# Performance work log

Hardware: AMD Instinct MI355X
Metric: run time of the kernel (lower is better)

The kernel has to match this reference:

```python
import jax, jax.numpy as jnp
import numpy as np

MAX_MARKER = 16


def setup_inputs() -> dict:
    key = jax.random.key(0)
    ks = jax.random.split(key, 7)
    B, W, H = 65536, 512, 8
    s1 = 1.0 / np.sqrt(W)
    s2 = 1.0 / np.sqrt(H)
    return {
        "x": jax.random.normal(ks[0], (B, W), dtype=jnp.float32),
        "W1": jax.random.uniform(ks[1], (H, W), jnp.float32, -s1, s1),
        "b1": jax.random.uniform(ks[2], (H,), jnp.float32, -s1, s1),
        "W2": jax.random.uniform(ks[3], (H, H), jnp.float32, -s2, s2),
        "b2": jax.random.uniform(ks[4], (H,), jnp.float32, -s2, s2),
        "W3": jax.random.uniform(ks[5], (W, H), jnp.float32, -s2, s2),
        "b3": jax.random.uniform(ks[6], (W,), jnp.float32, -s2, s2),
    }


def reference(x, W1, b1, W2, b2, W3, b3):
    # tiny MLP: window -> 8 -> 8 -> window
    h = jax.nn.relu(x @ W1.T + b1)
    h = jax.nn.relu(h @ W2.T + b2)
    y = h @ W3.T + b3
    p = jax.nn.softmax(y, axis=1)
    # force endpoints on (x.data[:,0]=1; x.data[:,-1]=1)
    p = p.at[:, 0].set(1.0).at[:, -1].set(1.0)
    # top-k along dim 1; threshold = min of the top-k values per row
    top_vals, _ = jax.lax.top_k(p, MAX_MARKER)
    thr = top_vals[:, -1:]  # sorted desc -> last is min, shape [B,1]
    # binary mask writes: >= thr -> 1, else 0
    return jnp.where(p >= thr, 1.0, 0.0).astype(p.dtype)
```

## Files before the change

kernel.cpp:

```cpp
#include <hip/hip_runtime.h>
#include <math.h>

#define B_ROWS 65536
#define WDIM 512
#define HDIM 8
#define THREADS 512

typedef float native_float4 __attribute__((ext_vector_type(4)));

template<int CTRL, int ROWM>
__device__ __forceinline__ float dpp_mov(float oldv, float x) {
    return __int_as_float(__builtin_amdgcn_update_dpp(
        __float_as_int(oldv), __float_as_int(x), CTRL, ROWM, 0xF, false));
}

__device__ __forceinline__ float wave_sum(float x) {
    x += dpp_mov<0x121, 0xF>(0.f, x);
    x += dpp_mov<0x122, 0xF>(0.f, x);
    x += dpp_mov<0x124, 0xF>(0.f, x);
    x += dpp_mov<0x128, 0xF>(0.f, x);
    x += dpp_mov<0x142, 0xA>(0.f, x);
    x += dpp_mov<0x143, 0xC>(0.f, x);
    return __int_as_float(__builtin_amdgcn_readlane(__float_as_int(x), 63));
}

__device__ __forceinline__ float wave_max(float x) {
    x = fmaxf(x, dpp_mov<0x121, 0xF>(-INFINITY, x));
    x = fmaxf(x, dpp_mov<0x122, 0xF>(-INFINITY, x));
    x = fmaxf(x, dpp_mov<0x124, 0xF>(-INFINITY, x));
    x = fmaxf(x, dpp_mov<0x128, 0xF>(-INFINITY, x));
    x = fmaxf(x, dpp_mov<0x142, 0xA>(-INFINITY, x));
    x = fmaxf(x, dpp_mov<0x143, 0xC>(-INFINITY, x));
    return __int_as_float(__builtin_amdgcn_readlane(__float_as_int(x), 63));
}

__device__ __forceinline__ float dot8(native_float4 a0, native_float4 a1,
                                      native_float4 b0, native_float4 b1) {
    float s = a0.x * b0.x;
    s = fmaf(a0.y, b0.y, s); s = fmaf(a0.z, b0.z, s); s = fmaf(a0.w, b0.w, s);
    s = fmaf(a1.x, b1.x, s); s = fmaf(a1.y, b1.y, s);
    s = fmaf(a1.z, b1.z, s); s = fmaf(a1.w, b1.w, s);
    return s;
}

__global__ __launch_bounds__(THREADS, 2)
void fused_mlp_topk(const float* __restrict__ x,
                    const float* __restrict__ W1,
                    const float* __restrict__ b1,
                    const float* __restrict__ W2,
                    const float* __restrict__ b2,
                    const float* __restrict__ W3,
                    const float* __restrict__ b3,
                    float* __restrict__ out)
{
    __shared__ __align__(16) float sW1[HDIM * WDIM];
    __shared__ __align__(16) float sW3t[HDIM * WDIM];
    __shared__ __align__(16) float sb3[WDIM];

    const int tid = threadIdx.x;
    for (int i = tid; i < HDIM * WDIM; i += THREADS) sW1[i] = W1[i];
    for (int i = tid; i < HDIM * WDIM; i += THREADS) {
        int r = i >> 3, k = i & 7;
        sW3t[k * WDIM + r] = W3[i];
    }
    for (int i = tid; i < WDIM; i += THREADS) sb3[i] = b3[i];
    __syncthreads();

    const int lane = tid & 63;
    const int wave_id = blockIdx.x * (THREADS / 64) + (tid >> 6);

    const native_float4* sW1v = reinterpret_cast<const native_float4*>(sW1);
    const native_float4* sW3v = reinterpret_cast<const native_float4*>(sW3t);
    const native_float4* sb3v = reinterpret_cast<const native_float4*>(sb3);

    int ra = wave_id * 2;
    const native_float4* xpa = reinterpret_cast<const native_float4*>(x + (size_t)ra * WDIM);
    const native_float4* xpb = xpa + (WDIM / 4);
    native_float4 xa0 = __builtin_nontemporal_load(xpa + lane);
    native_float4 xa1 = __builtin_nontemporal_load(xpa + lane + 64);
    native_float4 xb0 = __builtin_nontemporal_load(xpb + lane);
    native_float4 xb1 = __builtin_nontemporal_load(xpb + lane + 64);

    #pragma unroll 1
    for (int it = 0; it < 4; ++it) {
        float pa[HDIM], pb[HDIM];
        #pragma unroll
        for (int j = 0; j < HDIM; ++j) {
            native_float4 w0 = sW1v[j * 128 + lane];
            native_float4 w1 = sW1v[j * 128 + lane + 64];
            pa[j] = dot8(xa0, xa1, w0, w1);
            pb[j] = dot8(xb0, xb1, w0, w1);
        }
        float h1a[HDIM], h1b[HDIM];
        #pragma unroll
        for (int j = 0; j < HDIM; ++j) {
            float sa = wave_sum(pa[j]) + b1[j];
            float sb = wave_sum(pb[j]) + b1[j];
            h1a[j] = sa > 0.f ? sa : 0.f;
            h1b[j] = sb > 0.f ? sb : 0.f;
        }

        float h2a[HDIM], h2b[HDIM];
        #pragma unroll
        for (int j = 0; j < HDIM; ++j) {
            float va = b2[j], vb = b2[j];
            #pragma unroll
            for (int k = 0; k < HDIM; ++k) {
                const float w = W2[j * HDIM + k];
                va = fmaf(w, h1a[k], va);
                vb = fmaf(w, h1b[k], vb);
            }
            h2a[j] = va > 0.f ? va : 0.f;
            h2b[j] = vb > 0.f ? vb : 0.f;
        }

        native_float4 ya0 = sb3v[lane];
        native_float4 ya1 = sb3v[lane + 64];
        native_float4 yb0 = ya0, yb1 = ya1;
        #pragma unroll
        for (int k = 0; k < HDIM; ++k) {
            const float ha = h2a[k], hb = h2b[k];
            native_float4 w0 = sW3v[k * 128 + lane];
            native_float4 w1 = sW3v[k * 128 + lane + 64];
            ya0.x = fmaf(ha, w0.x, ya0.x); ya0.y = fmaf(ha, w0.y, ya0.y);
            ya0.z = fmaf(ha, w0.z, ya0.z); ya0.w = fmaf(ha, w0.w, ya0.w);
            ya1.x = fmaf(ha, w1.x, ya1.x); ya1.y = fmaf(ha, w1.y, ya1.y);
            ya1.z = fmaf(ha, w1.z, ya1.z); ya1.w = fmaf(ha, w1.w, ya1.w);
            yb0.x = fmaf(hb, w0.x, yb0.x); yb0.y = fmaf(hb, w0.y, yb0.y);
            yb0.z = fmaf(hb, w0.z, yb0.z); yb0.w = fmaf(hb, w0.w, yb0.w);
            yb1.x = fmaf(hb, w1.x, yb1.x); yb1.y = fmaf(hb, w1.y, yb1.y);
            yb1.z = fmaf(hb, w1.z, yb1.z); yb1.w = fmaf(hb, w1.w, yb1.w);
        }

        const int nra = ra + 16384;
        native_float4 nxa0, nxa1, nxb0, nxb1;
        if (it < 3) {
            const native_float4* nxpa = reinterpret_cast<const native_float4*>(x + (size_t)nra * WDIM);
            const native_float4* nxpb = nxpa + (WDIM / 4);
            nxa0 = __builtin_nontemporal_load(nxpa + lane);
            nxa1 = __builtin_nontemporal_load(nxpa + lane + 64);
            nxb0 = __builtin_nontemporal_load(nxpb + lane);
            nxb1 = __builtin_nontemporal_load(nxpb + lane + 64);
        }

        float lma = fmaxf(fmaxf(fmaxf(ya0.x, ya0.y), fmaxf(ya0.z, ya0.w)),
                          fmaxf(fmaxf(ya1.x, ya1.y), fmaxf(ya1.z, ya1.w)));
        float lmb = fmaxf(fmaxf(fmaxf(yb0.x, yb0.y), fmaxf(yb0.z, yb0.w)),
                          fmaxf(fmaxf(yb1.x, yb1.y), fmaxf(yb1.z, yb1.w)));
        float ma = wave_max(lma);
        float mb = wave_max(lmb);

        float ea[8], eb[8];
        ea[0] = expf(ya0.x - ma); ea[1] = expf(ya0.y - ma);
        ea[2] = expf(ya0.z - ma); ea[3] = expf(ya0.w - ma);
        ea[4] = expf(ya1.x - ma); ea[5] = expf(ya1.y - ma);
        ea[6] = expf(ya1.z - ma); ea[7] = expf(ya1.w - ma);
        eb[0] = expf(yb0.x - mb); eb[1] = expf(yb0.y - mb);
        eb[2] = expf(yb0.z - mb); eb[3] = expf(yb0.w - mb);
        eb[4] = expf(yb1.x - mb); eb[5] = expf(yb1.y - mb);
        eb[6] = expf(yb1.z - mb); eb[7] = expf(yb1.w - mb);
        float lsa = ((ea[0] + ea[1]) + (ea[2] + ea[3])) + ((ea[4] + ea[5]) + (ea[6] + ea[7]));
        float lsb = ((eb[0] + eb[1]) + (eb[2] + eb[3])) + ((eb[4] + eb[5]) + (eb[6] + eb[7]));
        float sa = wave_sum(lsa);
        float sb = wave_sum(lsb);

        float p_a[8], p_b[8];
        #pragma unroll
        for (int t = 0; t < 8; ++t) { p_a[t] = ea[t] / sa; p_b[t] = eb[t] / sb; }
        if (lane == 0)  { p_a[0] = 1.0f; p_b[0] = 1.0f; }
        if (lane == 63) { p_a[7] = 1.0f; p_b[7] = 1.0f; }

        unsigned Ua = 0x30000000u, Ub = 0x30000000u;
        for (int b = 27; b >= 0; --b) {
            const unsigned bit = 1u << b;
            const float cfa = __uint_as_float(Ua | bit);
            const float cfb = __uint_as_float(Ub | bit);
            int ca = 0, cb = 0;
            #pragma unroll
            for (int t = 0; t < 8; ++t) {
                ca += __popcll(__ballot(p_a[t] > cfa));
                cb += __popcll(__ballot(p_b[t] > cfb));
            }
            if (ca >= 16) Ua |= bit;
            if (cb >= 16) Ub |= bit;
        }
        const float thra = __uint_as_float(Ua + 1u);
        const float thrb = __uint_as_float(Ub + 1u);

        native_float4 r0, r1, q0, q1;
        r0.x = p_a[0] >= thra ? 1.f : 0.f;  r0.y = p_a[1] >= thra ? 1.f : 0.f;
        r0.z = p_a[2] >= thra ? 1.f : 0.f;  r0.w = p_a[3] >= thra ? 1.f : 0.f;
        r1.x = p_a[4] >= thra ? 1.f : 0.f;  r1.y = p_a[5] >= thra ? 1.f : 0.f;
        r1.z = p_a[6] >= thra ? 1.f : 0.f;  r1.w = p_a[7] >= thra ? 1.f : 0.f;
        q0.x = p_b[0] >= thrb ? 1.f : 0.f;  q0.y = p_b[1] >= thrb ? 1.f : 0.f;
        q0.z = p_b[2] >= thrb ? 1.f : 0.f;  q0.w = p_b[3] >= thrb ? 1.f : 0.f;
        q1.x = p_b[4] >= thrb ? 1.f : 0.f;  q1.y = p_b[5] >= thrb ? 1.f : 0.f;
        q1.z = p_b[6] >= thrb ? 1.f : 0.f;  q1.w = p_b[7] >= thrb ? 1.f : 0.f;

        native_float4* oa = reinterpret_cast<native_float4*>(out + (size_t)ra * WDIM);
        native_float4* ob = oa + (WDIM / 4);
        __builtin_nontemporal_store(r0, oa + lane);
        __builtin_nontemporal_store(r1, oa + lane + 64);
        __builtin_nontemporal_store(q0, ob + lane);
        __builtin_nontemporal_store(q1, ob + lane + 64);

        ra = nra;
        xa0 = nxa0; xa1 = nxa1; xb0 = nxb0; xb1 = nxb1;
    }
}

extern "C" void kernel_launch(void* const* d_in, const int* in_sizes, int n_in,
                              void* d_out, int out_size, void* d_ws, size_t ws_size,
                              hipStream_t stream) {
    const float* x  = (const float*)d_in[0];
    const float* W1 = (const float*)d_in[1];
    const float* b1 = (const float*)d_in[2];
    const float* W2 = (const float*)d_in[3];
    const float* b2 = (const float*)d_in[4];
    const float* W3 = (const float*)d_in[5];
    const float* b3 = (const float*)d_in[6];
    float* out = (float*)d_out;

    fused_mlp_topk<<<dim3(1024), dim3(THREADS), 0, stream>>>(x, W1, b1, W2, b2, W3, b3, out);
}
```

Baseline: 355.7 us.

## Process one row per wave per iteration and drop software prefetch for occupancy

Each wave now handles one row per iteration over 8 iterations instead of two interleaved rows over 4, and the explicit next-iteration prefetch of x is removed. Launch bounds rise from 2 to 4 blocks per CU so the register budget shrinks and more waves can be resident. The aim is to hide global-memory latency through occupancy rather than through per-wave ILP and prefetching. In exchange, the serial 28-step ballot threshold search and the wave reductions lose the two-row interleaving, and LDS use per block (about 34 KB) may cap residency anyway.

```diff
diff --git a/kernel.cpp b/kernel.cpp
--- a/kernel.cpp
+++ b/kernel.cpp
@@ -43,7 +43,7 @@
     return s;
 }
 
-__global__ __launch_bounds__(THREADS, 2)
+__global__ __launch_bounds__(THREADS, 4)
 void fused_mlp_topk(const float* __restrict__ x,
                     const float* __restrict__ W1,
                     const float* __restrict__ b1,
@@ -73,139 +73,93 @@
     const native_float4* sW3v = reinterpret_cast<const native_float4*>(sW3t);
     const native_float4* sb3v = reinterpret_cast<const native_float4*>(sb3);
 
-    int ra = wave_id * 2;
-    const native_float4* xpa = reinterpret_cast<const native_float4*>(x + (size_t)ra * WDIM);
-    const native_float4* xpb = xpa + (WDIM / 4);
-    native_float4 xa0 = __builtin_nontemporal_load(xpa + lane);
-    native_float4 xa1 = __builtin_nontemporal_load(xpa + lane + 64);
-    native_float4 xb0 = __builtin_nontemporal_load(xpb + lane);
-    native_float4 xb1 = __builtin_nontemporal_load(xpb + lane + 64);
+    int ra = wave_id;
 
     #pragma unroll 1
-    for (int it = 0; it < 4; ++it) {
-        float pa[HDIM], pb[HDIM];
+    for (int it = 0; it < 8; ++it) {
+        const native_float4* xp = reinterpret_cast<const native_float4*>(x + (size_t)ra * WDIM);
+        native_float4 x0 = __builtin_nontemporal_load(xp + lane);
+        native_float4 x1 = __builtin_nontemporal_load(xp + lane + 64);
+
+        float pa[HDIM];
         #pragma unroll
         for (int j = 0; j < HDIM; ++j) {
             native_float4 w0 = sW1v[j * 128 + lane];
             native_float4 w1 = sW1v[j * 128 + lane + 64];
-            pa[j] = dot8(xa0, xa1, w0, w1);
-            pb[j] = dot8(xb0, xb1, w0, w1);
+            pa[j] = dot8(x0, x1, w0, w1);
         }
-        float h1a[HDIM], h1b[HDIM];
+        float h1[HDIM];
         #pragma unroll
         for (int j = 0; j < HDIM; ++j) {
             float sa = wave_sum(pa[j]) + b1[j];
-            float sb = wave_sum(pb[j]) + b1[j];
-            h1a[j] = sa > 0.f ? sa : 0.f;
-            h1b[j] = sb > 0.f ? sb : 0.f;
+            h1[j] = sa > 0.f ? sa : 0.f;
         }
 
-        float h2a[HDIM], h2b[HDIM];
+        float h2[HDIM];
         #pragma unroll
         for (int j = 0; j < HDIM; ++j) {
-            float va = b2[j], vb = b2[j];
+            float va = b2[j];
             #pragma unroll
             for (int k = 0; k < HDIM; ++k) {
                 const float w = W2[j * HDIM + k];
-                va = fmaf(w, h1a[k], va);
-                vb = fmaf(w, h1b[k], vb);
+                va = fmaf(w, h1[k], va);
             }
-            h2a[j] = va > 0.f ? va : 0.f;
-            h2b[j] = vb > 0.f ? vb : 0.f;
+            h2[j] = va > 0.f ? va : 0.f;
         }
 
-        native_float4 ya0 = sb3v[lane];
-        native_float4 ya1 = sb3v[lane + 64];
-        native_float4 yb0 = ya0, yb1 = ya1;
+        native_float4 y0 = sb3v[lane];
+        native_float4 y1 = sb3v[lane + 64];
         #pragma unroll
         for (int k = 0; k < HDIM; ++k) {
-            const float ha = h2a[k], hb = h2b[k];
+            const float ha = h2[k];
             native_float4 w0 = sW3v[k * 128 + lane];
             native_float4 w1 = sW3v[k * 128 + lane + 64];
-            ya0.x = fmaf(ha, w0.x, ya0.x); ya0.y = fmaf(ha, w0.y, ya0.y);
-            ya0.z = fmaf(ha, w0.z, ya0.z); ya0.w = fmaf(ha, w0.w, ya0.w);
-            ya1.x = fmaf(ha, w1.x, ya1.x); ya1.y = fmaf(ha, w1.y, ya1.y);
-            ya1.z = fmaf(ha, w1.z, ya1.z); ya1.w = fmaf(ha, w1.w, ya1.w);
-            yb0.x = fmaf(hb, w0.x, yb0.x); yb0.y = fmaf(hb, w0.y, yb0.y);
-            yb0.z = fmaf(hb, w0.z, yb0.z); yb0.w = fmaf(hb, w0.w, yb0.w);
-            yb1.x = fmaf(hb, w1.x, yb1.x); yb1.y = fmaf(hb, w1.y, yb1.y);
-            yb1.z = fmaf(hb, w1.z, yb1.z); yb1.w = fmaf(hb, w1.w, yb1.w);
+            y0.x = fmaf(ha, w0.x, y0.x); y0.y = fmaf(ha, w0.y, y0.y);
+            y0.z = fmaf(ha, w0.z, y0.z); y0.w = fmaf(ha, w0.w, y0.w);
+            y1.x = fmaf(ha, w1.x, y1.x); y1.y = fmaf(ha, w1.y, y1.y);
+            y1.z = fmaf(ha, w1.z, y1.z); y1.w = fmaf(ha, w1.w, y1.w);
         }
 
-        const int nra = ra + 16384;
-        native_float4 nxa0, nxa1, nxb0, nxb1;
-        if (it < 3) {
-            const native_float4* nxpa = reinterpret_cast<const native_float4*>(x + (size_t)nra * WDIM);
-            const native_float4* nxpb = nxpa + (WDIM / 4);
-            nxa0 = __builtin_nontemporal_load(nxpa + lane);
-            nxa1 = __builtin_nontemporal_load(nxpa + lane + 64);
-            nxb0 = __builtin_nontemporal_load(nxpb + lane);
-            nxb1 = __builtin_nontemporal_load(nxpb + lane + 64);
-        }
+        float lma = fmaxf(fmaxf(fmaxf(y0.x, y0.y), fmaxf(y0.z, y0.w)),
+                          fmaxf(fmaxf(y1.x, y1.y), fmaxf(y1.z, y1.w)));
+        float ma = wave_max(lma);
 
-        float lma = fmaxf(fmaxf(fmaxf(ya0.x, ya0.y), fmaxf(ya0.z, ya0.w)),
-                          fmaxf(fmaxf(ya1.x, ya1.y), fmaxf(ya1.z, ya1.w)));
-        float lmb = fmaxf(fmaxf(fmaxf(yb0.x, yb0.y), fmaxf(yb0.z, yb0.w)),
-                          fmaxf(fmaxf(yb1.x, yb1.y), fmaxf(yb1.z, yb1.w)));
-        float ma = wave_max(lma);
-        float mb = wave_max(lmb);
+        float p[8];
+        p[0] = expf(y0.x - ma); p[1] = expf(y0.y - ma);
+        p[2] = expf(y0.z - ma); p[3] = expf(y0.w - ma);
+        p[4] = expf(y1.x - ma); p[5] = expf(y1.y - ma);
+        p[6] = expf(y1.z - ma); p[7] = expf(y1.w - ma);
+        float lsa = ((p[0] + p[1]) + (p[2] + p[3])) + ((p[4] + p[5]) + (p[6] + p[7]));
+        float sa = wave_sum(lsa);
 
-        float ea[8], eb[8];
-        ea[0] = expf(ya0.x - ma); ea[1] = expf(ya0.y - ma);
-        ea[2] = expf(ya0.z - ma); ea[3] = expf(ya0.w - ma);
-        ea[4] = expf(ya1.x - ma); ea[5] = expf(ya1.y - ma);
-        ea[6] = expf(ya1.z - ma); ea[7] = expf(ya1.w - ma);
-        eb[0] = expf(yb0.x - mb); eb[1] = expf(yb0.y - mb);
-        eb[2] = expf(yb0.z - mb); eb[3] = expf(yb0.w - mb);
-        eb[4] = expf(yb1.x - mb); eb[5] = expf(yb1.y - mb);
-        eb[6] = expf(yb1.z - mb); eb[7] = expf(yb1.w - mb);
-        float lsa = ((ea[0] + ea[1]) + (ea[2] + ea[3])) + ((ea[4] + ea[5]) + (ea[6] + ea[7]));
-        float lsb = ((eb[0] + eb[1]) + (eb[2] + eb[3])) + ((eb[4] + eb[5]) + (eb[6] + eb[7]));
-        float sa = wave_sum(lsa);
-        float sb = wave_sum(lsb);
+        #pragma unroll
+        for (int t = 0; t < 8; ++t) p[t] = p[t] / sa;
+        if (lane == 0)  p[0] = 1.0f;
+        if (lane == 63) p[7] = 1.0f;
 
-        float p_a[8], p_b[8];
-        #pragma unroll
-        for (int t = 0; t < 8; ++t) { p_a[t] = ea[t] / sa; p_b[t] = eb[t] / sb; }
-        if (lane == 0)  { p_a[0] = 1.0f; p_b[0] = 1.0f; }
-        if (lane == 63) { p_a[7] = 1.0f; p_b[7] = 1.0f; }
-
-        unsigned Ua = 0x30000000u, Ub = 0x30000000u;
+        unsigned Ua = 0x30000000u;
         for (int b = 27; b >= 0; --b) {
             const unsigned bit = 1u << b;
             const float cfa = __uint_as_float(Ua | bit);
-            const float cfb = __uint_as_float(Ub | bit);
-            int ca = 0, cb = 0;
+            int ca = 0;
             #pragma unroll
-            for (int t = 0; t < 8; ++t) {
-                ca += __popcll(__ballot(p_a[t] > cfa));
-                cb += __popcll(__ballot(p_b[t] > cfb));
-            }
+            for (int t = 0; t < 8; ++t)
+                ca += __popcll(__ballot(p[t] > cfa));
             if (ca >= 16) Ua |= bit;
-            if (cb >= 16) Ub |= bit;
         }
         const float thra = __uint_as_float(Ua + 1u);
-        const float thrb = __uint_as_float(Ub + 1u);
 
-        native_float4 r0, r1, q0, q1;
-        r0.x = p_a[0] >= thra ? 1.f : 0.f;  r0.y = p_a[1] >= thra ? 1.f : 0.f;
-        r0.z = p_a[2] >= thra ? 1.f : 0.f;  r0.w = p_a[3] >= thra ? 1.f : 0.f;
-        r1.x = p_a[4] >= thra ? 1.f : 0.f;  r1.y = p_a[5] >= thra ? 1.f : 0.f;
-        r1.z = p_a[6] >= thra ? 1.f : 0.f;  r1.w = p_a[7] >= thra ? 1.f : 0.f;
-        q0.x = p_b[0] >= thrb ? 1.f : 0.f;  q0.y = p_b[1] >= thrb ? 1.f : 0.f;
-        q0.z = p_b[2] >= thrb ? 1.f : 0.f;  q0.w = p_b[3] >= thrb ? 1.f : 0.f;
-        q1.x = p_b[4] >= thrb ? 1.f : 0.f;  q1.y = p_b[5] >= thrb ? 1.f : 0.f;
-        q1.z = p_b[6] >= thrb ? 1.f : 0.f;  q1.w = p_b[7] >= thrb ? 1.f : 0.f;
+        native_float4 r0, r1;
+        r0.x = p[0] >= thra ? 1.f : 0.f;  r0.y = p[1] >= thra ? 1.f : 0.f;
+        r0.z = p[2] >= thra ? 1.f : 0.f;  r0.w = p[3] >= thra ? 1.f : 0.f;
+        r1.x = p[4] >= thra ? 1.f : 0.f;  r1.y = p[5] >= thra ? 1.f : 0.f;
+        r1.z = p[6] >= thra ? 1.f : 0.f;  r1.w = p[7] >= thra ? 1.f : 0.f;
 
         native_float4* oa = reinterpret_cast<native_float4*>(out + (size_t)ra * WDIM);
-        native_float4* ob = oa + (WDIM / 4);
         __builtin_nontemporal_store(r0, oa + lane);
         __builtin_nontemporal_store(r1, oa + lane + 64);
-        __builtin_nontemporal_store(q0, ob + lane);
-        __builtin_nontemporal_store(q1, ob + lane + 64);
 
-        ra = nra;
-        xa0 = nxa0; xa1 = nxa1; xb0 = nxb0; xb1 = nxb1;
+        ra += 8192;
     }
 }
 
```

New measurement: 402.7 us. 13.2% more time.
